# Performance work log

Measured on AMD Instinct MI355X. Metric: run time of the kernel, lower is better.

## Reference

```python
import jax, jax.numpy as jnp
import numpy as np

N, F_IN, C, H, L = 4096, 768, 256, 4, 2
DH = C // H  # 64 per-head dim for GATv2


def _ln(x, g, b, eps=1e-5):
    mu = x.mean(-1, keepdims=True)
    var = ((x - mu) ** 2).mean(-1, keepdims=True)
    return (x - mu) / jnp.sqrt(var + eps) * g + b


def _gat_layer(x, wl, wr, att, b, src, dst):
    # GATv2Conv: e_ij = att . leaky_relu(Wl x_j + Wr x_i); softmax over incoming j; concat heads.
    xs = (x @ wl).reshape(N, H, DH)  # source transform
    xd = (x @ wr).reshape(N, H, DH)  # target transform
    e = jnp.einsum('ehd,hd->eh', jax.nn.leaky_relu(xs[src] + xd[dst], 0.2), att)  # [E,H]
    m = jax.ops.segment_max(e, dst, num_segments=N)          # segment softmax (stable)
    p = jnp.exp(e - m[dst])
    s = jax.ops.segment_sum(p, dst, num_segments=N)
    alpha = p / (s[dst] + 1e-16)                             # [E,H]
    out = jax.ops.segment_sum(alpha[:, :, None] * xs[src], dst, num_segments=N)
    return out.reshape(N, C) + b


def _mha(x, wq, wk, wv, bq, bk, bv, wo, bo):
    # nn.MultiheadAttention, batch=1 sequence of all news nodes, eval mode.
    q = (x @ wq + bq).reshape(N, H, DH)
    k = (x @ wk + bk).reshape(N, H, DH)
    v = (x @ wv + bv).reshape(N, H, DH)
    scale = np.float32(1.0 / np.sqrt(DH))
    a = jax.nn.softmax(jnp.einsum('nhd,mhd->hnm', q, k) * scale, axis=-1)  # [H,N,N]
    o = jnp.einsum('hnm,mhd->nhd', a, v).reshape(N, C)
    return o @ wo + bo


def setup_inputs() -> dict:
    key = jax.random.key(0)
    ks = jax.random.split(key, 32)
    rn = lambda k, shp: (jax.random.normal(k, shp, dtype=jnp.float32) * 0.02)
    inp = {
        'x': jax.random.normal(ks[0], (N, F_IN), dtype=jnp.float32),
        'edge_index': jax.random.randint(ks[1], (2, N * 64), 0, N, dtype=jnp.int64),
        'emb_w': rn(ks[2], (F_IN, C)), 'emb_b': jnp.zeros((C,), jnp.float32),
        'g1_wl': rn(ks[3], (C, C)), 'g1_wr': rn(ks[4], (C, C)),
        'g1_att': rn(ks[5], (H, DH)), 'g1_b': jnp.zeros((C,), jnp.float32),
        'g2_wl': rn(ks[6], (C, C)), 'g2_wr': rn(ks[7], (C, C)),
        'g2_att': rn(ks[8], (H, DH)), 'g2_b': jnp.zeros((C,), jnp.float32),
        'mha_wq': rn(ks[9], (C, C)), 'mha_wk': rn(ks[10], (C, C)), 'mha_wv': rn(ks[11], (C, C)),
        'mha_bq': jnp.zeros((C,), jnp.float32), 'mha_bk': jnp.zeros((C,), jnp.float32),
        'mha_bv': jnp.zeros((C,), jnp.float32),
        'mha_wo': rn(ks[12], (C, C)), 'mha_bo': jnp.zeros((C,), jnp.float32),
        'ln_g': jnp.ones((C,), jnp.float32), 'ln_b': jnp.zeros((C,), jnp.float32),
        'cls_w1': rn(ks[13], (C, C // 2)), 'cls_b1': jnp.zeros((C // 2,), jnp.float32),
        'cls_w2': rn(ks[14], (C // 2, 2)), 'cls_b2': jnp.zeros((2,), jnp.float32),
    }
    return inp


def reference(x, edge_index, emb_w, emb_b, g1_wl, g1_wr, g1_att, g1_b,
              g2_wl, g2_wr, g2_att, g2_b, mha_wq, mha_wk, mha_wv, mha_bq,
              mha_bk, mha_bv, mha_wo, mha_bo, ln_g, ln_b,
              cls_w1, cls_b1, cls_w2, cls_b2):
    # add self loops (GATv2Conv default add_self_loops=True)
    loops = jnp.arange(N, dtype=edge_index.dtype)
    src = jnp.concatenate([edge_index[0], loops])
    dst = jnp.concatenate([edge_index[1], loops])

    h = x @ emb_w + emb_b                              # node embedding Linear(-1, C)
    h = jax.nn.relu(_gat_layer(h, g1_wl, g1_wr, g1_att, g1_b, src, dst))
    h = jax.nn.relu(_gat_layer(h, g2_wl, g2_wr, g2_att, g2_b, src, dst))

    # entity-aware self-attention + residual LayerNorm
    enh = _mha(h, mha_wq, mha_wk, mha_wv, mha_bq, mha_bk, mha_bv, mha_wo, mha_bo)
    h = _ln(h + enh, ln_g, ln_b)

    # classifier MLP (dropout = identity in eval)
    h = jax.nn.relu(h @ cls_w1 + cls_b1)
    return h @ cls_w2 + cls_b2
```

## Files before the change

kernel.cpp:

```cpp
#include <hip/hip_runtime.h>

typedef __attribute__((ext_vector_type(8))) short short8_t;
typedef __attribute__((ext_vector_type(4))) float f32x4_t;

#define N_NODES  4096
#define E0_EDGES 262144
#define E_TOTAL  266240
#define SPLITS   8
#define KV_PER_SPLIT (N_NODES / SPLITS)

__device__ __forceinline__ float bf2f(unsigned short u){
  union { unsigned int i; float f; } v; v.i = ((unsigned int)u) << 16; return v.f;
}
__device__ __forceinline__ unsigned short f2bf(float f){
  union { float f; unsigned int i; } v; v.f = f;
  unsigned int r = (v.i + 0x7FFFu + ((v.i >> 16) & 1u)) >> 16;
  return (unsigned short)r;
}
__device__ __forceinline__ unsigned int cvtpk_bf16(float lo, float hi){
  unsigned int r;
  asm volatile("v_cvt_pk_bf16_f32 %0, %1, %2" : "=v"(r) : "v"(lo), "v"(hi));
  return r;
}
template<int CTRL>
__device__ __forceinline__ float dpp_add(float x){
  int v = __builtin_amdgcn_update_dpp(0, __float_as_int(x), CTRL, 0xF, 0xF, true);
  return x + __int_as_float(v);
}
__device__ __forceinline__ float rowsum16(float x){
  x = dpp_add<0xB1>(x); x = dpp_add<0x4E>(x); x = dpp_add<0x124>(x); x = dpp_add<0x128>(x);
  return x;
}
__device__ __forceinline__ void wg_barrier(){
  asm volatile("s_waitcnt lgkmcnt(0)" ::: "memory");
  __builtin_amdgcn_s_barrier();
  asm volatile("" ::: "memory");
}

struct TJob { const float* src; unsigned short* dst; int rows, cols, tile0; };
struct TJobs { TJob j[10]; };

__global__ __launch_bounds__(256) void prep_kernel(const float* __restrict__ x, unsigned short* __restrict__ xb,
                                                   TJobs jobs, int tb, int* __restrict__ zp){
  __shared__ unsigned short tile[64 * 64];
  int b = blockIdx.x, t = threadIdx.x;
  if (b < 3072){
    int i = (b * 256 + t) * 4;
    float4 v = *(const float4*)&x[i];
    union { unsigned short u[4]; uint2 q; } o;
    o.u[0] = f2bf(v.x); o.u[1] = f2bf(v.y); o.u[2] = f2bf(v.z); o.u[3] = f2bf(v.w);
    *(uint2*)&xb[i] = o.q;
    return;
  }
  if (b < 3072 + tb){
    int bb = b - 3072;
    int ji = 0;
    #pragma unroll
    for (int k = 1; k < 10; k++) if (bb >= jobs.j[k].tile0) ji = k;
    TJob J = jobs.j[ji];
    int lt = bb - J.tile0;
    int tpr = J.cols >> 6;
    int tr = lt / tpr, tc = lt - tr * tpr;
    #pragma unroll
    for (int i2 = 0; i2 < 2; i2++){
      int e = i2 * 2048 + t * 8;
      int nl = e >> 6, c8 = e & 63;
      const float* sp = &J.src[(size_t)(tr * 64 + nl) * J.cols + tc * 64 + c8];
      float4 v0 = *(const float4*)sp;
      float4 v1 = *(const float4*)(sp + 4);
      union { unsigned short u[8]; uint4 q; } o;
      o.u[0]=f2bf(v0.x); o.u[1]=f2bf(v0.y); o.u[2]=f2bf(v0.z); o.u[3]=f2bf(v0.w);
      o.u[4]=f2bf(v1.x); o.u[5]=f2bf(v1.y); o.u[6]=f2bf(v1.z); o.u[7]=f2bf(v1.w);
      *(uint4*)&tile[nl * 64 + (((c8 >> 3) ^ ((nl >> 3) & 7)) * 8)] = o.q;
    }
    __syncthreads();
    #pragma unroll
    for (int i2 = 0; i2 < 2; i2++){
      int e = i2 * 2048 + t * 8;
      int cl = e >> 6, n8 = e & 63;
      union { unsigned short u[8]; uint4 q; } o;
      #pragma unroll
      for (int j = 0; j < 8; j++){
        int row = n8 + j;
        o.u[j] = tile[row * 64 + (((cl >> 3) ^ ((row >> 3) & 7)) * 8) + (cl & 7)];
      }
      *(uint4*)&J.dst[(size_t)(tc * 64 + cl) * J.rows + tr * 64 + n8] = o.q;
    }
    return;
  }
  int i = (b - 3072 - tb) * 256 + t;
  if (i < 8192) zp[i] = 0;
}

__global__ __launch_bounds__(256) void scatter_kernel(const int* __restrict__ ei, const int* __restrict__ offs,
                                                      int* __restrict__ cur, int* __restrict__ csrc){
  int e = blockIdx.x * 256 + threadIdx.x;
  if (e >= E_TOTAL) return;
  int s, d;
  if (e < E0_EDGES){ s = ei[e]; d = ei[E0_EDGES + e]; }
  else { s = d = e - E0_EDGES; }
  int pos = offs[d] + atomicAdd(&cur[d], 1);
  csrc[pos] = s;
}

struct GJob { const unsigned short* Wt; const float* bias; float* outF; unsigned short* outB; unsigned short* outT; };
struct GJobs { GJob j[3]; };
struct AuxJob { int mode; const int* ei; int* a; int* b; };

__global__ __launch_bounds__(256) void gemm_kernel(const unsigned short* __restrict__ A, GJobs jobs,
                                                   int K, int Nc, int relu, AuxJob AX){
  __shared__ unsigned short lds[8192];
  const int t = threadIdx.x;

  if (AX.mode && blockIdx.z == gridDim.z - 1){
    int flat = blockIdx.x + (blockIdx.y << 6);
    if (AX.mode == 1){
      for (int e = flat * 256 + t; e < E_TOTAL; e += 65536){
        int d = (e < E0_EDGES) ? AX.ei[E0_EDGES + e] : (e - E0_EDGES);
        atomicAdd(&AX.a[d], 1);
      }
    } else if (flat == 0){
      int* wtot = (int*)lds;
      int lane = t & 63, w = t >> 6;
      int v[16];
      int base = t * 16;
      int s = 0;
      #pragma unroll
      for (int j = 0; j < 16; j++){ v[j] = AX.a[base + j]; s += v[j]; }
      int x = s;
      #pragma unroll
      for (int off = 1; off < 64; off <<= 1){
        int y = __shfl_up(x, off, 64);
        if (lane >= off) x += y;
      }
      if (lane == 63) wtot[w] = x;
      __syncthreads();
      int wbase = 0;
      #pragma unroll
      for (int k = 0; k < 4; k++) if (k < w) wbase += wtot[k];
      int run = wbase + x - s;
      #pragma unroll
      for (int j = 0; j < 16; j++){ AX.b[base + j] = run; run += v[j]; }
      if (t == 255) AX.b[N_NODES] = run;
    }
    return;
  }

  const GJob job = jobs.j[blockIdx.z];
  const int lane = t & 63, w = t >> 6;
  const int wm = w >> 1, wn = w & 1;
  const int c16 = lane & 15, g = lane >> 4;
  const int bm = blockIdx.x, bn = blockIdx.y;

  const int srow = t >> 2, schunk = t & 3;
  const unsigned short* Ag = A      + (size_t)(bm * 64 + srow) * K + schunk * 8;
  const unsigned short* Bg = job.Wt + (size_t)(bn * 64 + srow) * K + schunk * 8;
  const int swz = srow * 32 + ((schunk ^ ((srow >> 1) & 3)) * 8);

  const int arow0 = wm * 32 + c16, arow1 = arow0 + 16;
  const int aoff0 = arow0 * 32 + ((g ^ ((arow0 >> 1) & 3)) * 8);
  const int aoff1 = arow1 * 32 + ((g ^ ((arow1 >> 1) & 3)) * 8);
  const int bcol0 = wn * 32 + c16, bcol1 = bcol0 + 16;
  const int boff0 = 2048 + bcol0 * 32 + ((g ^ ((bcol0 >> 1) & 3)) * 8);
  const int boff1 = 2048 + bcol1 * 32 + ((g ^ ((bcol1 >> 1) & 3)) * 8);

  f32x4_t acc[2][2] = {};
  const int nk = K >> 5;

  {
    uint4 av = *(const uint4*)(Ag);
    uint4 bv = *(const uint4*)(Bg);
    *(uint4*)&lds[swz]        = av;
    *(uint4*)&lds[2048 + swz] = bv;
  }
  int cur = 0;
  for (int i = 0; i < nk; i++){
    const bool pf = (i + 1) < nk;
    uint4 av, bv;
    if (pf){
      av = *(const uint4*)(Ag + (i + 1) * 32);
      bv = *(const uint4*)(Bg + (i + 1) * 32);
    }
    wg_barrier();
    const int base = cur * 4096;
    union { uint4 u; short8_t s; } a0, a1, b0, b1;
    a0.u = *(const uint4*)&lds[base + aoff0];
    a1.u = *(const uint4*)&lds[base + aoff1];
    b0.u = *(const uint4*)&lds[base + boff0];
    b1.u = *(const uint4*)&lds[base + boff1];
    acc[0][0] = __builtin_amdgcn_mfma_f32_16x16x32_bf16(a0.s, b0.s, acc[0][0], 0, 0, 0);
    acc[0][1] = __builtin_amdgcn_mfma_f32_16x16x32_bf16(a0.s, b1.s, acc[0][1], 0, 0, 0);
    acc[1][0] = __builtin_amdgcn_mfma_f32_16x16x32_bf16(a1.s, b0.s, acc[1][0], 0, 0, 0);
    acc[1][1] = __builtin_amdgcn_mfma_f32_16x16x32_bf16(a1.s, b1.s, acc[1][1], 0, 0, 0);
    if (pf){
      const int nb = (cur ^ 1) * 4096;
      *(uint4*)&lds[nb + swz]        = av;
      *(uint4*)&lds[nb + 2048 + swz] = bv;
      cur ^= 1;
    }
  }

  #pragma unroll
  for (int fm = 0; fm < 2; fm++){
    #pragma unroll
    for (int fn = 0; fn < 2; fn++){
      int col = bn * 64 + wn * 32 + fn * 16 + c16;
      float bia = job.bias ? job.bias[col] : 0.f;
      float vv[4];
      #pragma unroll
      for (int r = 0; r < 4; r++){
        float v = acc[fm][fn][r] + bia;
        if (relu) v = fmaxf(v, 0.f);
        vv[r] = v;
      }
      int row0 = bm * 64 + wm * 32 + fm * 16 + g * 4;
      if (job.outF){
        #pragma unroll
        for (int r = 0; r < 4; r++) job.outF[(size_t)(row0 + r) * Nc + col] = vv[r];
      }
      if (job.outB){
        #pragma unroll
        for (int r = 0; r < 4; r++) job.outB[(size_t)(row0 + r) * Nc + col] = f2bf(vv[r]);
      }
      if (job.outT){
        union { unsigned short u[4]; uint2 q; } pk;
        #pragma unroll
        for (int r = 0; r < 4; r++) pk.u[r] = f2bf(vv[r]);
        *(uint2*)&job.outT[(size_t)col * 4096 + row0] = pk.q;
      }
    }
  }
}

__global__ __launch_bounds__(256) void gat_gather(const unsigned short* __restrict__ xs, const unsigned short* __restrict__ xd,
                                                  const float* __restrict__ att, const float* __restrict__ bias,
                                                  const int* __restrict__ offs, const int* __restrict__ csrc,
                                                  unsigned short* __restrict__ outB, float* __restrict__ outF){
  __shared__ float combL[4][256];
  __shared__ float combS[4][4];
  const int i = blockIdx.x, t = threadIdx.x;
  const int lane = t & 63, w = t >> 6;
  float xdc[4], attc[4];
  {
    uint2 xv = *(const uint2*)&xd[i * 256 + lane * 4];
    xdc[0] = bf2f((unsigned short)(xv.x & 0xffff)); xdc[1] = bf2f((unsigned short)(xv.x >> 16));
    xdc[2] = bf2f((unsigned short)(xv.y & 0xffff)); xdc[3] = bf2f((unsigned short)(xv.y >> 16));
    float4 av = *(const float4*)&att[lane * 4];
    attc[0] = av.x; attc[1] = av.y; attc[2] = av.z; attc[3] = av.w;
  }
  const int b0 = offs[i], b1 = offs[i + 1];
  float acc0 = 0.f, acc1 = 0.f, acc2 = 0.f, acc3 = 0.f, ssum = 0.f;
  int p = b0 + w;
  for (; p + 4 < b1; p += 8){
    int sA = csrc[p], sB = csrc[p + 4];
    uint2 xa = *(const uint2*)&xs[sA * 256 + lane * 4];
    uint2 xb = *(const uint2*)&xs[sB * 256 + lane * 4];
    float a0 = bf2f((unsigned short)(xa.x & 0xffff)), a1 = bf2f((unsigned short)(xa.x >> 16));
    float a2 = bf2f((unsigned short)(xa.y & 0xffff)), a3 = bf2f((unsigned short)(xa.y >> 16));
    float b0_ = bf2f((unsigned short)(xb.x & 0xffff)), b1_ = bf2f((unsigned short)(xb.x >> 16));
    float b2_ = bf2f((unsigned short)(xb.y & 0xffff)), b3_ = bf2f((unsigned short)(xb.y >> 16));
    float va0 = a0 + xdc[0]; va0 = (va0 > 0.f) ? va0 : 0.2f * va0;
    float va1 = a1 + xdc[1]; va1 = (va1 > 0.f) ? va1 : 0.2f * va1;
    float va2 = a2 + xdc[2]; va2 = (va2 > 0.f) ? va2 : 0.2f * va2;
    float va3 = a3 + xdc[3]; va3 = (va3 > 0.f) ? va3 : 0.2f * va3;
    float vb0 = b0_ + xdc[0]; vb0 = (vb0 > 0.f) ? vb0 : 0.2f * vb0;
    float vb1 = b1_ + xdc[1]; vb1 = (vb1 > 0.f) ? vb1 : 0.2f * vb1;
    float vb2 = b2_ + xdc[2]; vb2 = (vb2 > 0.f) ? vb2 : 0.2f * vb2;
    float vb3 = b3_ + xdc[3]; vb3 = (vb3 > 0.f) ? vb3 : 0.2f * vb3;
    float eA = rowsum16(va0 * attc[0] + va1 * attc[1] + va2 * attc[2] + va3 * attc[3]);
    float eB = rowsum16(vb0 * attc[0] + vb1 * attc[1] + vb2 * attc[2] + vb3 * attc[3]);
    float pA = __expf(eA), pB = __expf(eB);
    ssum += pA + pB;
    acc0 += pA * a0 + pB * b0_; acc1 += pA * a1 + pB * b1_;
    acc2 += pA * a2 + pB * b2_; acc3 += pA * a3 + pB * b3_;
  }
  if (p < b1){
    int s = csrc[p];
    uint2 xv = *(const uint2*)&xs[s * 256 + lane * 4];
    float x0 = bf2f((unsigned short)(xv.x & 0xffff)), x1 = bf2f((unsigned short)(xv.x >> 16));
    float x2 = bf2f((unsigned short)(xv.y & 0xffff)), x3 = bf2f((unsigned short)(xv.y >> 16));
    float v0 = x0 + xdc[0]; v0 = (v0 > 0.f) ? v0 : 0.2f * v0;
    float v1 = x1 + xdc[1]; v1 = (v1 > 0.f) ? v1 : 0.2f * v1;
    float v2 = x2 + xdc[2]; v2 = (v2 > 0.f) ? v2 : 0.2f * v2;
    float v3 = x3 + xdc[3]; v3 = (v3 > 0.f) ? v3 : 0.2f * v3;
    float e = rowsum16(v0 * attc[0] + v1 * attc[1] + v2 * attc[2] + v3 * attc[3]);
    float pe = __expf(e);
    ssum += pe;
    acc0 += pe * x0; acc1 += pe * x1; acc2 += pe * x2; acc3 += pe * x3;
  }
  combL[w][lane * 4 + 0] = acc0; combL[w][lane * 4 + 1] = acc1;
  combL[w][lane * 4 + 2] = acc2; combL[w][lane * 4 + 3] = acc3;
  if ((lane & 15) == 0) combS[w][lane >> 4] = ssum;
  __syncthreads();
  float atot = combL[0][t] + combL[1][t] + combL[2][t] + combL[3][t];
  int hh = t >> 6;
  float stot = combS[0][hh] + combS[1][hh] + combS[2][hh] + combS[3][hh];
  float o = atot / (stot + 1e-16f) + bias[t];
  o = fmaxf(o, 0.f);
  outB[i * 256 + t] = f2bf(o);
  if (outF) outF[i * 256 + t] = o;
}

__global__ __launch_bounds__(512, 2) void attn_kernel(const unsigned short* __restrict__ qb, const unsigned short* __restrict__ kb,
                                                      const unsigned short* __restrict__ vt,
                                                      float* __restrict__ Opart, float* __restrict__ Ol){
  __shared__ unsigned short K_lds[2][4096];
  __shared__ unsigned short V_lds[2][4096];
  __shared__ unsigned short P_lds[8][2048];
  const int t = threadIdx.x, lane = t & 63, w = t >> 6;
  const int c16 = lane & 15, g = lane >> 4;
  const int h = blockIdx.y, bq = blockIdx.x, sp = blockIdx.z;

  const int sr = t >> 3, sc = (t & 7) * 8;
  const int kw = sr * 64 + (((t & 7) ^ ((sr >> 1) & 7)) * 8);
  const int vw = sr * 64 + (((t & 7) ^ (sr & 7)) * 8);

  short8_t qa[2][2];
  #pragma unroll
  for (int qm = 0; qm < 2; qm++){
    int qrow = bq * 256 + w * 32 + qm * 16 + c16;
    union { uint4 u; short8_t s; } cv0, cv1;
    cv0.u = *(const uint4*)&qb[(size_t)qrow * 256 + h * 64 + g * 8];
    cv1.u = *(const uint4*)&qb[(size_t)qrow * 256 + h * 64 + 32 + g * 8];
    qa[qm][0] = cv0.s; qa[qm][1] = cv1.s;
  }

  f32x4_t oacc[2][4] = {};
  float lsum[2] = {0.f, 0.f};

  const int kv_lo = sp * KV_PER_SPLIT;
  {
    uint4 k0 = *(const uint4*)&kb[(size_t)(kv_lo + sr) * 256 + h * 64 + sc];
    uint4 v0 = *(const uint4*)&vt[(size_t)(h * 64 + sr) * 4096 + kv_lo + sc];
    *(uint4*)&K_lds[0][kw] = k0;
    *(uint4*)&V_lds[0][vw] = v0;
  }
  int cur = 0;

  for (int ti = 0; ti < KV_PER_SPLIT / 64; ti++){
    const bool pf = (ti + 1) < KV_PER_SPLIT / 64;
    uint4 nk, nv;
    if (pf){
      int kvn = kv_lo + (ti + 1) * 64;
      nk = *(const uint4*)&kb[(size_t)(kvn + sr) * 256 + h * 64 + sc];
      nv = *(const uint4*)&vt[(size_t)(h * 64 + sr) * 4096 + kvn + sc];
    }
    wg_barrier();
    const unsigned short* Kb = K_lds[cur];
    const unsigned short* Vb = V_lds[cur];
    unsigned short* Pw = P_lds[w];

    f32x4_t sacc[2][4] = {};
    #pragma unroll
    for (int kd = 0; kd < 2; kd++){
      #pragma unroll
      for (int fn = 0; fn < 4; fn++){
        union { uint4 u; short8_t s; } kf;
        kf.u = *(const uint4*)&Kb[(fn * 16 + c16) * 64 + (((kd * 4 + g) ^ ((c16 >> 1) & 7)) * 8)];
        sacc[0][fn] = __builtin_amdgcn_mfma_f32_16x16x32_bf16(kf.s, qa[0][kd], sacc[0][fn], 0, 0, 0);
        sacc[1][fn] = __builtin_amdgcn_mfma_f32_16x16x32_bf16(kf.s, qa[1][kd], sacc[1][fn], 0, 0, 0);
      }
    }

    #pragma unroll
    for (int qm = 0; qm < 2; qm++){
      float ps = 0.f;
      int row = qm * 16 + c16;
      #pragma unroll
      for (int fn = 0; fn < 4; fn++){
        float p0 = __expf(sacc[qm][fn][0] * 0.125f);
        float p1 = __expf(sacc[qm][fn][1] * 0.125f);
        float p2 = __expf(sacc[qm][fn][2] * 0.125f);
        float p3 = __expf(sacc[qm][fn][3] * 0.125f);
        ps += (p0 + p1) + (p2 + p3);
        uint2 pk;
        pk.x = cvtpk_bf16(p0, p1);
        pk.y = cvtpk_bf16(p2, p3);
        int chunk = (fn * 2 + (g >> 1)) ^ (c16 & 7);
        *(uint2*)&Pw[row * 64 + chunk * 8 + (g & 1) * 4] = pk;
      }
      ps += __shfl_xor(ps, 16, 64);
      ps += __shfl_xor(ps, 32, 64);
      lsum[qm] += ps;
    }

    #pragma unroll
    for (int kd2 = 0; kd2 < 2; kd2++){
      const int ch = (((kd2 * 4 + g) ^ (c16 & 7)) * 8);
      union { uint4 u; short8_t s; } pt0, pt1;
      pt0.u = *(const uint4*)&Pw[c16 * 64 + ch];
      pt1.u = *(const uint4*)&Pw[(16 + c16) * 64 + ch];
      #pragma unroll
      for (int fn = 0; fn < 4; fn++){
        union { uint4 u; short8_t s; } vf;
        vf.u = *(const uint4*)&Vb[(fn * 16 + c16) * 64 + ch];
        oacc[0][fn] = __builtin_amdgcn_mfma_f32_16x16x32_bf16(vf.s, pt0.s, oacc[0][fn], 0, 0, 0);
        oacc[1][fn] = __builtin_amdgcn_mfma_f32_16x16x32_bf16(vf.s, pt1.s, oacc[1][fn], 0, 0, 0);
      }
    }

    if (pf){
      *(uint4*)&K_lds[cur ^ 1][kw] = nk;
      *(uint4*)&V_lds[cur ^ 1][vw] = nv;
      cur ^= 1;
    }
  }

  const int sh = sp * 4 + h;
  #pragma unroll
  for (int qm = 0; qm < 2; qm++){
    int node = bq * 256 + w * 32 + qm * 16 + c16;
    #pragma unroll
    for (int fn = 0; fn < 4; fn++){
      *(float4*)&Opart[((size_t)sh * N_NODES + node) * 64 + fn * 16 + g * 4] =
        *(float4*)&oacc[qm][fn];
    }
    if (g == 0) Ol[(size_t)sh * N_NODES + node] = lsum[qm];
  }
}

__global__ __launch_bounds__(256) void wo_ln_kernel(const float* __restrict__ Opart, const float* __restrict__ Ol,
                                                    const unsigned short* __restrict__ Wt, const float* __restrict__ bo,
                                                    const float* __restrict__ h2f, const float* __restrict__ gg,
                                                    const float* __restrict__ bb, unsigned short* __restrict__ outB){
  __shared__ unsigned short Ab[2][512];
  __shared__ unsigned short Bb[2][8192];
  __shared__ float red1[4][16], red2[4][16];
  __shared__ float Ls[64];
  const int t = threadIdx.x, lane = t & 63, w = t >> 6;
  const int c16 = lane & 15, g = lane >> 4;
  const int bm = blockIdx.x;

  const int arow = t >> 2, achk = t & 3;
  const int aswz = arow * 32 + ((achk ^ ((arow >> 1) & 3)) * 8);
  const int bq_ = t >> 2, bchk = t & 3;

  if (t < 64){
    int node = bm * 16 + (t >> 2), h = t & 3;
    float L = 0.f;
    #pragma unroll
    for (int s = 0; s < SPLITS; s++) L += Ol[(size_t)(s * 4 + h) * N_NODES + node];
    Ls[t] = 1.f / L;
  }
  __syncthreads();

  const int afr = c16 * 32 + ((g ^ ((c16 >> 1) & 3)) * 8);
  int bfr[4];
  #pragma unroll
  for (int fn = 0; fn < 4; fn++){
    int col = w * 64 + fn * 16 + c16;
    bfr[fn] = col * 32 + ((g ^ ((col >> 1) & 3)) * 8);
  }

  const int anode = bm * 16 + arow;
  auto loadA = [&](int k0, float4* pa){
    int c0 = k0 + achk * 8;
    int hh = c0 >> 6, d0 = c0 & 63;
    #pragma unroll
    for (int s = 0; s < SPLITS; s++){
      const float* bp = &Opart[((size_t)(s * 4 + hh) * N_NODES + anode) * 64 + d0];
      pa[s * 2]     = *(const float4*)bp;
      pa[s * 2 + 1] = *(const float4*)(bp + 4);
    }
  };
  auto packA = [&](int k0, const float4* pa) -> uint4 {
    float a[8] = {0.f,0.f,0.f,0.f,0.f,0.f,0.f,0.f};
    #pragma unroll
    for (int s = 0; s < SPLITS; s++){
      a[0] += pa[s*2].x;   a[1] += pa[s*2].y;   a[2] += pa[s*2].z;   a[3] += pa[s*2].w;
      a[4] += pa[s*2+1].x; a[5] += pa[s*2+1].y; a[6] += pa[s*2+1].z; a[7] += pa[s*2+1].w;
    }
    int c0 = k0 + achk * 8;
    float Li = Ls[(arow << 2) | (c0 >> 6)];
    union { unsigned short u[8]; uint4 q; } o;
    #pragma unroll
    for (int j = 0; j < 8; j++) o.u[j] = f2bf(a[j] * Li);
    return o.q;
  };

  f32x4_t acc[4] = {};
  {
    if (t < 64){
      float4 pa0[SPLITS * 2];
      loadA(0, pa0);
      *(uint4*)&Ab[0][aswz] = packA(0, pa0);
    }
    #pragma unroll
    for (int j = 0; j < 4; j++){
      int col = j * 64 + bq_;
      *(uint4*)&Bb[0][col * 32 + ((bchk ^ ((col >> 1) & 3)) * 8)] = *(const uint4*)&Wt[(size_t)col * 256 + bchk * 8];
    }
  }
  int cur = 0;
  for (int i = 0; i < 8; i++){
    const bool pf = i < 7;
    float4 pa[SPLITS * 2]; uint4 pb[4];
    int k1 = (i + 1) * 32;
    if (pf){
      if (t < 64) loadA(k1, pa);
      #pragma unroll
      for (int j = 0; j < 4; j++){
        int col = j * 64 + bq_;
        pb[j] = *(const uint4*)&Wt[(size_t)col * 256 + k1 + bchk * 8];
      }
    }
    wg_barrier();
    union { uint4 u; short8_t s; } a, b;
    a.u = *(const uint4*)&Ab[cur][afr];
    #pragma unroll
    for (int fn = 0; fn < 4; fn++){
      b.u = *(const uint4*)&Bb[cur][bfr[fn]];
      acc[fn] = __builtin_amdgcn_mfma_f32_16x16x32_bf16(a.s, b.s, acc[fn], 0, 0, 0);
    }
    if (pf){
      if (t < 64) *(uint4*)&Ab[cur ^ 1][aswz] = packA(k1, pa);
      #pragma unroll
      for (int j = 0; j < 4; j++){
        int col = j * 64 + bq_;
        *(uint4*)&Bb[cur ^ 1][col * 32 + ((bchk ^ ((col >> 1) & 3)) * 8)] = pb[j];
      }
      cur ^= 1;
    }
  }

  float vv[4][4];
  #pragma unroll
  for (int fn = 0; fn < 4; fn++){
    int col = w * 64 + fn * 16 + c16;
    float bia = bo[col];
    #pragma unroll
    for (int r = 0; r < 4; r++)
      vv[fn][r] = acc[fn][r] + bia + h2f[(size_t)(bm * 16 + g * 4 + r) * 256 + col];
  }
  #pragma unroll
  for (int r = 0; r < 4; r++){
    float a = 0.f, b = 0.f;
    #pragma unroll
    for (int fn = 0; fn < 4; fn++){ a += vv[fn][r]; b += vv[fn][r] * vv[fn][r]; }
    a = rowsum16(a); b = rowsum16(b);
    if (c16 == 0){ red1[w][g * 4 + r] = a; red2[w][g * 4 + r] = b; }
  }
  __syncthreads();
  #pragma unroll
  for (int r = 0; r < 4; r++){
    int row = g * 4 + r;
    float S1 = red1[0][row] + red1[1][row] + red1[2][row] + red1[3][row];
    float S2 = red2[0][row] + red2[1][row] + red2[2][row] + red2[3][row];
    float mean = S1 * (1.f / 256.f);
    float var = S2 * (1.f / 256.f) - mean * mean;
    float rs = rsqrtf(var + 1e-5f);
    #pragma unroll
    for (int fn = 0; fn < 4; fn++){
      int col = w * 64 + fn * 16 + c16;
      outB[(size_t)(bm * 16 + row) * 256 + col] = f2bf((vv[fn][r] - mean) * rs * gg[col] + bb[col]);
    }
  }
}

__global__ __launch_bounds__(256) void cls_kernel(const unsigned short* __restrict__ hln,
                                                  const unsigned short* __restrict__ Wt1, const float* __restrict__ b1,
                                                  const float* __restrict__ w2, const float* __restrict__ b2,
                                                  float* __restrict__ out){
  __shared__ unsigned short Ab[2][512];
  __shared__ unsigned short Bb[2][4096];
  __shared__ float red0[4][16], red1[4][16];
  const int t = threadIdx.x, lane = t & 63, w = t >> 6;
  const int c16 = lane & 15, g = lane >> 4;
  const int bm = blockIdx.x;

  const int arow = t >> 2, achk = t & 3;
  const unsigned short* Agp = hln + (size_t)(bm * 16 + arow) * 256 + achk * 8;
  const int aswz = arow * 32 + ((achk ^ ((arow >> 1) & 3)) * 8);
  const int bq_ = t >> 2, bchk = t & 3;

  const int afr = c16 * 32 + ((g ^ ((c16 >> 1) & 3)) * 8);
  int bfr[2];
  #pragma unroll
  for (int fn = 0; fn < 2; fn++){
    int col = w * 32 + fn * 16 + c16;
    bfr[fn] = col * 32 + ((g ^ ((col >> 1) & 3)) * 8);
  }

  f32x4_t acc[2] = {};
  {
    if (t < 64) *(uint4*)&Ab[0][aswz] = *(const uint4*)Agp;
    #pragma unroll
    for (int j = 0; j < 2; j++){
      int col = j * 64 + bq_;
      *(uint4*)&Bb[0][col * 32 + ((bchk ^ ((col >> 1) & 3)) * 8)] = *(const uint4*)&Wt1[(size_t)col * 256 + bchk * 8];
    }
  }
  int cur = 0;
  for (int i = 0; i < 8; i++){
    const bool pf = i < 7;
    uint4 pa; uint4 pb[2];
    if (pf){
      int k1 = (i + 1) * 32;
      if (t < 64) pa = *(const uint4*)(Agp + k1);
      #pragma unroll
      for (int j = 0; j < 2; j++){
        int col = j * 64 + bq_;
        pb[j] = *(const uint4*)&Wt1[(size_t)col * 256 + k1 + bchk * 8];
      }
    }
    wg_barrier();
    union { uint4 u; short8_t s; } a, b;
    a.u = *(const uint4*)&Ab[cur][afr];
    #pragma unroll
    for (int fn = 0; fn < 2; fn++){
      b.u = *(const uint4*)&Bb[cur][bfr[fn]];
      acc[fn] = __builtin_amdgcn_mfma_f32_16x16x32_bf16(a.s, b.s, acc[fn], 0, 0, 0);
    }
    if (pf){
      if (t < 64) *(uint4*)&Ab[cur ^ 1][aswz] = pa;
      #pragma unroll
      for (int j = 0; j < 2; j++){
        int col = j * 64 + bq_;
        *(uint4*)&Bb[cur ^ 1][col * 32 + ((bchk ^ ((col >> 1) & 3)) * 8)] = pb[j];
      }
      cur ^= 1;
    }
  }

  float vv[2][4];
  #pragma unroll
  for (int fn = 0; fn < 2; fn++){
    int col = w * 32 + fn * 16 + c16;
    float bia = b1[col];
    #pragma unroll
    for (int r = 0; r < 4; r++) vv[fn][r] = fmaxf(acc[fn][r] + bia, 0.f);
  }
  float w20 = w2[(w * 32 + c16) * 2],      w21 = w2[(w * 32 + c16) * 2 + 1];
  float w30 = w2[(w * 32 + 16 + c16) * 2], w31 = w2[(w * 32 + 16 + c16) * 2 + 1];
  #pragma unroll
  for (int r = 0; r < 4; r++){
    float a0 = vv[0][r] * w20 + vv[1][r] * w30;
    float a1 = vv[0][r] * w21 + vv[1][r] * w31;
    a0 = rowsum16(a0); a1 = rowsum16(a1);
    if (c16 == 0){ red0[w][g * 4 + r] = a0; red1[w][g * 4 + r] = a1; }
  }
  __syncthreads();
  if (t < 16){
    float q0 = red0[0][t] + red0[1][t] + red0[2][t] + red0[3][t] + b2[0];
    float q1 = red1[0][t] + red1[1][t] + red1[2][t] + red1[3][t] + b2[1];
    out[(size_t)(bm * 16 + t) * 2]     = q0;
    out[(size_t)(bm * 16 + t) * 2 + 1] = q1;
  }
}

extern "C" void kernel_launch(void* const* d_in, const int* in_sizes, int n_in,
                              void* d_out, int out_size, void* d_ws, size_t ws_size,
                              hipStream_t stream){
  const float* x      = (const float*)d_in[0];
  const int*   ei     = (const int*)d_in[1];
  const float* emb_w  = (const float*)d_in[2];
  const float* emb_b  = (const float*)d_in[3];
  const float* g1_wl  = (const float*)d_in[4];
  const float* g1_wr  = (const float*)d_in[5];
  const float* g1_att = (const float*)d_in[6];
  const float* g1_b   = (const float*)d_in[7];
  const float* g2_wl  = (const float*)d_in[8];
  const float* g2_wr  = (const float*)d_in[9];
  const float* g2_att = (const float*)d_in[10];
  const float* g2_b   = (const float*)d_in[11];
  const float* wq     = (const float*)d_in[12];
  const float* wk     = (const float*)d_in[13];
  const float* wv     = (const float*)d_in[14];
  const float* bq     = (const float*)d_in[15];
  const float* bk     = (const float*)d_in[16];
  const float* bv     = (const float*)d_in[17];
  const float* wo     = (const float*)d_in[18];
  const float* bo     = (const float*)d_in[19];
  const float* ln_g   = (const float*)d_in[20];
  const float* ln_b   = (const float*)d_in[21];
  const float* cls_w1 = (const float*)d_in[22];
  const float* cls_b1 = (const float*)d_in[23];
  const float* cls_w2 = (const float*)d_in[24];
  const float* cls_b2 = (const float*)d_in[25];
  float* out = (float*)d_out;

  char* wsb = (char*)d_ws;
  size_t o = 0;
  auto take = [&](size_t bytes) -> char* {
    char* r = wsb + o; o += (bytes + 255) & ~(size_t)255; return r;
  };
  unsigned short* wt_emb  = (unsigned short*)take(768 * 256 * 2);
  unsigned short* wt_wl1  = (unsigned short*)take(256 * 256 * 2);
  unsigned short* wt_wr1  = (unsigned short*)take(256 * 256 * 2);
  unsigned short* wt_wl2  = (unsigned short*)take(256 * 256 * 2);
  unsigned short* wt_wr2  = (unsigned short*)take(256 * 256 * 2);
  unsigned short* wt_wq   = (unsigned short*)take(256 * 256 * 2);
  unsigned short* wt_wk   = (unsigned short*)take(256 * 256 * 2);
  unsigned short* wt_wv   = (unsigned short*)take(256 * 256 * 2);
  unsigned short* wt_wo   = (unsigned short*)take(256 * 256 * 2);
  unsigned short* wt_cls1 = (unsigned short*)take(256 * 128 * 2);
  unsigned short* x_bf    = (unsigned short*)take((size_t)4096 * 768 * 2);
  unsigned short* h0_bf   = (unsigned short*)take((size_t)4096 * 256 * 2);
  unsigned short* xs1_bf  = (unsigned short*)take((size_t)4096 * 256 * 2);
  unsigned short* xd1_bf  = (unsigned short*)take((size_t)4096 * 256 * 2);
  unsigned short* h1_bf   = (unsigned short*)take((size_t)4096 * 256 * 2);
  unsigned short* xs2_bf  = (unsigned short*)take((size_t)4096 * 256 * 2);
  unsigned short* xd2_bf  = (unsigned short*)take((size_t)4096 * 256 * 2);
  unsigned short* h2_bf   = (unsigned short*)take((size_t)4096 * 256 * 2);
  float*          h2_f    = (float*)take((size_t)4096 * 256 * 4);
  unsigned short* q_bf    = (unsigned short*)take((size_t)4096 * 256 * 2);
  unsigned short* k_bf    = (unsigned short*)take((size_t)4096 * 256 * 2);
  unsigned short* vt_bf   = (unsigned short*)take((size_t)4096 * 256 * 2);
  unsigned short* hln_bf  = (unsigned short*)take((size_t)4096 * 256 * 2);
  int* deg  = (int*)take(4096 * 4);
  int* cur  = (int*)take(4096 * 4);
  int* offs = (int*)take(4097 * 4);
  int* csrc = (int*)take((size_t)E_TOTAL * 4);
  float* Opart = (float*)take((size_t)SPLITS * 4 * N_NODES * 64 * 4);
  float* Ol    = (float*)take((size_t)SPLITS * 4 * N_NODES * 4);

  TJobs TJ;
  TJob tj[10] = {
    { emb_w,  wt_emb,  768, 256, 0 },
    { g1_wl,  wt_wl1,  256, 256, 0 },
    { g1_wr,  wt_wr1,  256, 256, 0 },
    { g2_wl,  wt_wl2,  256, 256, 0 },
    { g2_wr,  wt_wr2,  256, 256, 0 },
    { wq,     wt_wq,   256, 256, 0 },
    { wk,     wt_wk,   256, 256, 0 },
    { wv,     wt_wv,   256, 256, 0 },
    { wo,     wt_wo,   256, 256, 0 },
    { cls_w1, wt_cls1, 256, 128, 0 },
  };
  int tb = 0;
  for (int i = 0; i < 10; i++){
    tj[i].tile0 = tb;
    tb += (tj[i].rows >> 6) * (tj[i].cols >> 6);
    TJ.j[i] = tj[i];
  }
  prep_kernel<<<3072 + tb + 32, 256, 0, stream>>>(x, x_bf, TJ, tb, deg);

  GJobs J;
  AuxJob AX0 = { 0, nullptr, nullptr, nullptr };
  J = {}; J.j[0] = { wt_emb, emb_b, nullptr, h0_bf, nullptr };
  AuxJob AXh = { 1, ei, deg, nullptr };
  gemm_kernel<<<dim3(64, 4, 2), 256, 0, stream>>>(x_bf, J, 768, 256, 0, AXh);
  J = {}; J.j[0] = { wt_wl1, nullptr, nullptr, xs1_bf, nullptr }; J.j[1] = { wt_wr1, nullptr, nullptr, xd1_bf, nullptr };
  AuxJob AXs = { 2, nullptr, deg, offs };
  gemm_kernel<<<dim3(64, 4, 3), 256, 0, stream>>>(h0_bf, J, 256, 256, 0, AXs);
  scatter_kernel<<<(E_TOTAL + 255) / 256, 256, 0, stream>>>(ei, offs, cur, csrc);
  gat_gather<<<4096, 256, 0, stream>>>(xs1_bf, xd1_bf, g1_att, g1_b, offs, csrc, h1_bf, nullptr);
  J = {}; J.j[0] = { wt_wl2, nullptr, nullptr, xs2_bf, nullptr }; J.j[1] = { wt_wr2, nullptr, nullptr, xd2_bf, nullptr };
  gemm_kernel<<<dim3(64, 4, 2), 256, 0, stream>>>(h1_bf, J, 256, 256, 0, AX0);
  gat_gather<<<4096, 256, 0, stream>>>(xs2_bf, xd2_bf, g2_att, g2_b, offs, csrc, h2_bf, h2_f);
  J = {};
  J.j[0] = { wt_wq, bq, nullptr, q_bf, nullptr };
  J.j[1] = { wt_wk, bk, nullptr, k_bf, nullptr };
  J.j[2] = { wt_wv, bv, nullptr, nullptr, vt_bf };
  gemm_kernel<<<dim3(64, 4, 3), 256, 0, stream>>>(h2_bf, J, 256, 256, 0, AX0);
  attn_kernel<<<dim3(16, 4, SPLITS), 512, 0, stream>>>(q_bf, k_bf, vt_bf, Opart, Ol);
  wo_ln_kernel<<<256, 256, 0, stream>>>(Opart, Ol, wt_wo, bo, h2_f, ln_g, ln_b, hln_bf);
  cls_kernel<<<256, 256, 0, stream>>>(hln_bf, wt_cls1, cls_b1, cls_w2, cls_b2, out);

  (void)in_sizes; (void)n_in; (void)out_size; (void)ws_size;
}
```

Measured before the change: 164.1 us.

## Keep attention probabilities in registers, fold Q scale, fuse LN with classifier

The attention kernel now feeds the bf16 probabilities straight from registers into 16x16x16 MFMAs instead of staging them through LDS. The block shrinks to 256 threads with 128 query rows each, and the 1/sqrt(d) scale is moved into the Q projection epilogue. The Wo+LayerNorm kernel is fused with the classifier MLP, keeping the normalized rows in LDS instead of a global round trip and dropping one launch. The narrower K=16 MFMA issues more instructions, and halving the query tile means each K/V tile is reused across fewer queries.

```diff
diff --git a/kernel.cpp b/kernel.cpp
--- a/kernel.cpp
+++ b/kernel.cpp
@@ -1,6 +1,7 @@
 #include <hip/hip_runtime.h>
 
 typedef __attribute__((ext_vector_type(8))) short short8_t;
+typedef __attribute__((ext_vector_type(4))) short short4_t;
 typedef __attribute__((ext_vector_type(4))) float f32x4_t;
 
 #define N_NODES  4096
@@ -35,6 +36,10 @@
   asm volatile("s_waitcnt lgkmcnt(0)" ::: "memory");
   __builtin_amdgcn_s_barrier();
   asm volatile("" ::: "memory");
+}
+__device__ __forceinline__ f32x4_t mfma16(short4_t a, short4_t b, f32x4_t c){
+  asm("v_mfma_f32_16x16x16_bf16 %0, %1, %2, %0" : "+v"(c) : "v"(a), "v"(b));
+  return c;
 }
 
 struct TJob { const float* src; unsigned short* dst; int rows, cols, tile0; };
@@ -103,7 +108,7 @@
   csrc[pos] = s;
 }
 
-struct GJob { const unsigned short* Wt; const float* bias; float* outF; unsigned short* outB; unsigned short* outT; };
+struct GJob { const unsigned short* Wt; const float* bias; float* outF; unsigned short* outB; unsigned short* outT; float scale; };
 struct GJobs { GJob j[3]; };
 struct AuxJob { int mode; const int* ei; int* a; int* b; };
 
@@ -209,7 +214,7 @@
       float vv[4];
       #pragma unroll
       for (int r = 0; r < 4; r++){
-        float v = acc[fm][fn][r] + bia;
+        float v = (acc[fm][fn][r] + bia) * job.scale;
         if (relu) v = fmaxf(v, 0.f);
         vv[r] = v;
       }
@@ -301,24 +306,27 @@
   if (outF) outF[i * 256 + t] = o;
 }
 
-__global__ __launch_bounds__(512, 2) void attn_kernel(const unsigned short* __restrict__ qb, const unsigned short* __restrict__ kb,
+__global__ __launch_bounds__(256, 4) void attn_kernel(const unsigned short* __restrict__ qb, const unsigned short* __restrict__ kb,
                                                       const unsigned short* __restrict__ vt,
                                                       float* __restrict__ Opart, float* __restrict__ Ol){
   __shared__ unsigned short K_lds[2][4096];
   __shared__ unsigned short V_lds[2][4096];
-  __shared__ unsigned short P_lds[8][2048];
   const int t = threadIdx.x, lane = t & 63, w = t >> 6;
   const int c16 = lane & 15, g = lane >> 4;
   const int h = blockIdx.y, bq = blockIdx.x, sp = blockIdx.z;
 
-  const int sr = t >> 3, sc = (t & 7) * 8;
-  const int kw = sr * 64 + (((t & 7) ^ ((sr >> 1) & 7)) * 8);
-  const int vw = sr * 64 + (((t & 7) ^ (sr & 7)) * 8);
+  const int e0 = t * 8, e1 = 2048 + t * 8;
+  const int sr0 = e0 >> 6, sc0 = e0 & 63;
+  const int sr1 = e1 >> 6, sc1 = e1 & 63;
+  const int kw0 = sr0 * 64 + (((sc0 >> 3) ^ ((sr0 >> 1) & 7)) * 8);
+  const int kw1 = sr1 * 64 + (((sc1 >> 3) ^ ((sr1 >> 1) & 7)) * 8);
+  const int vw0 = sr0 * 64 + (((sc0 >> 3) ^ (sr0 & 7)) * 8);
+  const int vw1 = sr1 * 64 + (((sc1 >> 3) ^ (sr1 & 7)) * 8);
 
   short8_t qa[2][2];
   #pragma unroll
   for (int qm = 0; qm < 2; qm++){
-    int qrow = bq * 256 + w * 32 + qm * 16 + c16;
+    int qrow = bq * 128 + w * 32 + qm * 16 + c16;
     union { uint4 u; short8_t s; } cv0, cv1;
     cv0.u = *(const uint4*)&qb[(size_t)qrow * 256 + h * 64 + g * 8];
     cv1.u = *(const uint4*)&qb[(size_t)qrow * 256 + h * 64 + 32 + g * 8];
@@ -330,25 +338,28 @@
 
   const int kv_lo = sp * KV_PER_SPLIT;
   {
-    uint4 k0 = *(const uint4*)&kb[(size_t)(kv_lo + sr) * 256 + h * 64 + sc];
-    uint4 v0 = *(const uint4*)&vt[(size_t)(h * 64 + sr) * 4096 + kv_lo + sc];
-    *(uint4*)&K_lds[0][kw] = k0;
-    *(uint4*)&V_lds[0][vw] = v0;
+    uint4 k0 = *(const uint4*)&kb[(size_t)(kv_lo + sr0) * 256 + h * 64 + sc0];
+    uint4 k1 = *(const uint4*)&kb[(size_t)(kv_lo + sr1) * 256 + h * 64 + sc1];
+    uint4 v0 = *(const uint4*)&vt[(size_t)(h * 64 + sr0) * 4096 + kv_lo + sc0];
+    uint4 v1 = *(const uint4*)&vt[(size_t)(h * 64 + sr1) * 4096 + kv_lo + sc1];
+    *(uint4*)&K_lds[0][kw0] = k0; *(uint4*)&K_lds[0][kw1] = k1;
+    *(uint4*)&V_lds[0][vw0] = v0; *(uint4*)&V_lds[0][vw1] = v1;
   }
   int cur = 0;
 
   for (int ti = 0; ti < KV_PER_SPLIT / 64; ti++){
     const bool pf = (ti + 1) < KV_PER_SPLIT / 64;
-    uint4 nk, nv;
+    uint4 nk0, nk1, nv0, nv1;
     if (pf){
       int kvn = kv_lo + (ti + 1) * 64;
-      nk = *(const uint4*)&kb[(size_t)(kvn + sr) * 256 + h * 64 + sc];
-      nv = *(const uint4*)&vt[(size_t)(h * 64 + sr) * 4096 + kvn + sc];
+      nk0 = *(const uint4*)&kb[(size_t)(kvn + sr0) * 256 + h * 64 + sc0];
+      nk1 = *(const uint4*)&kb[(size_t)(kvn + sr1) * 256 + h * 64 + sc1];
+      nv0 = *(const uint4*)&vt[(size_t)(h * 64 + sr0) * 4096 + kvn + sc0];
+      nv1 = *(const uint4*)&vt[(size_t)(h * 64 + sr1) * 4096 + kvn + sc1];
     }
     wg_barrier();
     const unsigned short* Kb = K_lds[cur];
     const unsigned short* Vb = V_lds[cur];
-    unsigned short* Pw = P_lds[w];
 
     f32x4_t sacc[2][4] = {};
     #pragma unroll
@@ -362,22 +373,21 @@
       }
     }
 
+    short4_t pfr[2][4];
     #pragma unroll
     for (int qm = 0; qm < 2; qm++){
       float ps = 0.f;
-      int row = qm * 16 + c16;
       #pragma unroll
       for (int fn = 0; fn < 4; fn++){
-        float p0 = __expf(sacc[qm][fn][0] * 0.125f);
-        float p1 = __expf(sacc[qm][fn][1] * 0.125f);
-        float p2 = __expf(sacc[qm][fn][2] * 0.125f);
-        float p3 = __expf(sacc[qm][fn][3] * 0.125f);
+        float p0 = __expf(sacc[qm][fn][0]);
+        float p1 = __expf(sacc[qm][fn][1]);
+        float p2 = __expf(sacc[qm][fn][2]);
+        float p3 = __expf(sacc[qm][fn][3]);
         ps += (p0 + p1) + (p2 + p3);
-        uint2 pk;
-        pk.x = cvtpk_bf16(p0, p1);
-        pk.y = cvtpk_bf16(p2, p3);
-        int chunk = (fn * 2 + (g >> 1)) ^ (c16 & 7);
-        *(uint2*)&Pw[row * 64 + chunk * 8 + (g & 1) * 4] = pk;
+        union { uint2 u; short4_t s; } pk;
+        pk.u.x = cvtpk_bf16(p0, p1);
+        pk.u.y = cvtpk_bf16(p2, p3);
+        pfr[qm][fn] = pk.s;
       }
       ps += __shfl_xor(ps, 16, 64);
       ps += __shfl_xor(ps, 32, 64);
@@ -385,23 +395,21 @@
     }
 
     #pragma unroll
-    for (int kd2 = 0; kd2 < 2; kd2++){
-      const int ch = (((kd2 * 4 + g) ^ (c16 & 7)) * 8);
-      union { uint4 u; short8_t s; } pt0, pt1;
-      pt0.u = *(const uint4*)&Pw[c16 * 64 + ch];
-      pt1.u = *(const uint4*)&Pw[(16 + c16) * 64 + ch];
-      #pragma unroll
-      for (int fn = 0; fn < 4; fn++){
-        union { uint4 u; short8_t s; } vf;
-        vf.u = *(const uint4*)&Vb[(fn * 16 + c16) * 64 + ch];
-        oacc[0][fn] = __builtin_amdgcn_mfma_f32_16x16x32_bf16(vf.s, pt0.s, oacc[0][fn], 0, 0, 0);
-        oacc[1][fn] = __builtin_amdgcn_mfma_f32_16x16x32_bf16(vf.s, pt1.s, oacc[1][fn], 0, 0, 0);
+    for (int fnkv = 0; fnkv < 4; fnkv++){
+      const int chb = fnkv * 2 + (g >> 1);
+      #pragma unroll
+      for (int fd = 0; fd < 4; fd++){
+        int row = fd * 16 + c16;
+        union { uint2 u; short4_t s; } vf;
+        vf.u = *(const uint2*)&Vb[row * 64 + ((chb ^ (row & 7)) * 8) + (g & 1) * 4];
+        oacc[0][fd] = mfma16(vf.s, pfr[0][fnkv], oacc[0][fd]);
+        oacc[1][fd] = mfma16(vf.s, pfr[1][fnkv], oacc[1][fd]);
       }
     }
 
     if (pf){
-      *(uint4*)&K_lds[cur ^ 1][kw] = nk;
-      *(uint4*)&V_lds[cur ^ 1][vw] = nv;
+      *(uint4*)&K_lds[cur ^ 1][kw0] = nk0; *(uint4*)&K_lds[cur ^ 1][kw1] = nk1;
+      *(uint4*)&V_lds[cur ^ 1][vw0] = nv0; *(uint4*)&V_lds[cur ^ 1][vw1] = nv1;
       cur ^= 1;
     }
   }
@@ -409,23 +417,29 @@
   const int sh = sp * 4 + h;
   #pragma unroll
   for (int qm = 0; qm < 2; qm++){
-    int node = bq * 256 + w * 32 + qm * 16 + c16;
-    #pragma unroll
-    for (int fn = 0; fn < 4; fn++){
-      *(float4*)&Opart[((size_t)sh * N_NODES + node) * 64 + fn * 16 + g * 4] =
-        *(float4*)&oacc[qm][fn];
+    int node = bq * 128 + w * 32 + qm * 16 + c16;
+    #pragma unroll
+    for (int fd = 0; fd < 4; fd++){
+      *(float4*)&Opart[((size_t)sh * N_NODES + node) * 64 + fd * 16 + g * 4] =
+        *(float4*)&oacc[qm][fd];
     }
     if (g == 0) Ol[(size_t)sh * N_NODES + node] = lsum[qm];
   }
 }
 
-__global__ __launch_bounds__(256) void wo_ln_kernel(const float* __restrict__ Opart, const float* __restrict__ Ol,
-                                                    const unsigned short* __restrict__ Wt, const float* __restrict__ bo,
-                                                    const float* __restrict__ h2f, const float* __restrict__ gg,
-                                                    const float* __restrict__ bb, unsigned short* __restrict__ outB){
+__global__ __launch_bounds__(256) void wo_ln_cls_kernel(const float* __restrict__ Opart, const float* __restrict__ Ol,
+                                                        const unsigned short* __restrict__ Wt, const float* __restrict__ bo,
+                                                        const float* __restrict__ h2f, const float* __restrict__ gg,
+                                                        const float* __restrict__ bb,
+                                                        const unsigned short* __restrict__ Wt1, const float* __restrict__ b1,
+                                                        const float* __restrict__ w2, const float* __restrict__ b2,
+                                                        float* __restrict__ out){
   __shared__ unsigned short Ab[2][512];
   __shared__ unsigned short Bb[2][8192];
+  __shared__ unsigned short Cb[2][4096];
+  __shared__ unsigned short hl[16 * 264];
   __shared__ float red1[4][16], red2[4][16];
+  __shared__ float cred0[4][16], cred1[4][16];
   __shared__ float Ls[64];
   const int t = threadIdx.x, lane = t & 63, w = t >> 6;
   const int c16 = lane & 15, g = lane >> 4;
@@ -552,51 +566,31 @@
     #pragma unroll
     for (int fn = 0; fn < 4; fn++){
       int col = w * 64 + fn * 16 + c16;
-      outB[(size_t)(bm * 16 + row) * 256 + col] = f2bf((vv[fn][r] - mean) * rs * gg[col] + bb[col]);
-    }
-  }
-}
-
-__global__ __launch_bounds__(256) void cls_kernel(const unsigned short* __restrict__ hln,
-                                                  const unsigned short* __restrict__ Wt1, const float* __restrict__ b1,
-                                                  const float* __restrict__ w2, const float* __restrict__ b2,
-                                                  float* __restrict__ out){
-  __shared__ unsigned short Ab[2][512];
-  __shared__ unsigned short Bb[2][4096];
-  __shared__ float red0[4][16], red1[4][16];
-  const int t = threadIdx.x, lane = t & 63, w = t >> 6;
-  const int c16 = lane & 15, g = lane >> 4;
-  const int bm = blockIdx.x;
-
-  const int arow = t >> 2, achk = t & 3;
-  const unsigned short* Agp = hln + (size_t)(bm * 16 + arow) * 256 + achk * 8;
-  const int aswz = arow * 32 + ((achk ^ ((arow >> 1) & 3)) * 8);
-  const int bq_ = t >> 2, bchk = t & 3;
-
-  const int afr = c16 * 32 + ((g ^ ((c16 >> 1) & 3)) * 8);
-  int bfr[2];
+      hl[row * 264 + col] = f2bf((vv[fn][r] - mean) * rs * gg[col] + bb[col]);
+    }
+  }
+
+  wg_barrier();
+  int cfr[2];
   #pragma unroll
   for (int fn = 0; fn < 2; fn++){
     int col = w * 32 + fn * 16 + c16;
-    bfr[fn] = col * 32 + ((g ^ ((col >> 1) & 3)) * 8);
-  }
-
-  f32x4_t acc[2] = {};
+    cfr[fn] = col * 32 + ((g ^ ((col >> 1) & 3)) * 8);
+  }
+  f32x4_t cacc[2] = {};
   {
-    if (t < 64) *(uint4*)&Ab[0][aswz] = *(const uint4*)Agp;
     #pragma unroll
     for (int j = 0; j < 2; j++){
       int col = j * 64 + bq_;
-      *(uint4*)&Bb[0][col * 32 + ((bchk ^ ((col >> 1) & 3)) * 8)] = *(const uint4*)&Wt1[(size_t)col * 256 + bchk * 8];
-    }
-  }
-  int cur = 0;
+      *(uint4*)&Cb[0][col * 32 + ((bchk ^ ((col >> 1) & 3)) * 8)] = *(const uint4*)&Wt1[(size_t)col * 256 + bchk * 8];
+    }
+  }
+  cur = 0;
   for (int i = 0; i < 8; i++){
     const bool pf = i < 7;
-    uint4 pa; uint4 pb[2];
+    uint4 pb[2];
     if (pf){
       int k1 = (i + 1) * 32;
-      if (t < 64) pa = *(const uint4*)(Agp + k1);
       #pragma unroll
       for (int j = 0; j < 2; j++){
         int col = j * 64 + bq_;
@@ -605,44 +599,42 @@
     }
     wg_barrier();
     union { uint4 u; short8_t s; } a, b;
-    a.u = *(const uint4*)&Ab[cur][afr];
+    a.u = *(const uint4*)&hl[c16 * 264 + i * 32 + g * 8];
     #pragma unroll
     for (int fn = 0; fn < 2; fn++){
-      b.u = *(const uint4*)&Bb[cur][bfr[fn]];
-      acc[fn] = __builtin_amdgcn_mfma_f32_16x16x32_bf16(a.s, b.s, acc[fn], 0, 0, 0);
+      b.u = *(const uint4*)&Cb[cur][cfr[fn]];
+      cacc[fn] = __builtin_amdgcn_mfma_f32_16x16x32_bf16(a.s, b.s, cacc[fn], 0, 0, 0);
     }
     if (pf){
-      if (t < 64) *(uint4*)&Ab[cur ^ 1][aswz] = pa;
       #pragma unroll
       for (int j = 0; j < 2; j++){
         int col = j * 64 + bq_;
-        *(uint4*)&Bb[cur ^ 1][col * 32 + ((bchk ^ ((col >> 1) & 3)) * 8)] = pb[j];
+        *(uint4*)&Cb[cur ^ 1][col * 32 + ((bchk ^ ((col >> 1) & 3)) * 8)] = pb[j];
       }
       cur ^= 1;
     }
   }
-
-  float vv[2][4];
+  float cv[2][4];
   #pragma unroll
   for (int fn = 0; fn < 2; fn++){
     int col = w * 32 + fn * 16 + c16;
     float bia = b1[col];
     #pragma unroll
-    for (int r = 0; r < 4; r++) vv[fn][r] = fmaxf(acc[fn][r] + bia, 0.f);
+    for (int r = 0; r < 4; r++) cv[fn][r] = fmaxf(cacc[fn][r] + bia, 0.f);
   }
   float w20 = w2[(w * 32 + c16) * 2],      w21 = w2[(w * 32 + c16) * 2 + 1];
   float w30 = w2[(w * 32 + 16 + c16) * 2], w31 = w2[(w * 32 + 16 + c16) * 2 + 1];
   #pragma unroll
   for (int r = 0; r < 4; r++){
-    float a0 = vv[0][r] * w20 + vv[1][r] * w30;
-    float a1 = vv[0][r] * w21 + vv[1][r] * w31;
+    float a0 = cv[0][r] * w20 + cv[1][r] * w30;
+    float a1 = cv[0][r] * w21 + cv[1][r] * w31;
     a0 = rowsum16(a0); a1 = rowsum16(a1);
-    if (c16 == 0){ red0[w][g * 4 + r] = a0; red1[w][g * 4 + r] = a1; }
+    if (c16 == 0){ cred0[w][g * 4 + r] = a0; cred1[w][g * 4 + r] = a1; }
   }
   __syncthreads();
   if (t < 16){
-    float q0 = red0[0][t] + red0[1][t] + red0[2][t] + red0[3][t] + b2[0];
-    float q1 = red1[0][t] + red1[1][t] + red1[2][t] + red1[3][t] + b2[1];
+    float q0 = cred0[0][t] + cred0[1][t] + cred0[2][t] + cred0[3][t] + b2[0];
+    float q1 = cred1[0][t] + cred1[1][t] + cred1[2][t] + cred1[3][t] + b2[1];
     out[(size_t)(bm * 16 + t) * 2]     = q0;
     out[(size_t)(bm * 16 + t) * 2 + 1] = q1;
   }
@@ -706,7 +698,6 @@
   unsigned short* q_bf    = (unsigned short*)take((size_t)4096 * 256 * 2);
   unsigned short* k_bf    = (unsigned short*)take((size_t)4096 * 256 * 2);
   unsigned short* vt_bf   = (unsigned short*)take((size_t)4096 * 256 * 2);
-  unsigned short* hln_bf  = (unsigned short*)take((size_t)4096 * 256 * 2);
   int* deg  = (int*)take(4096 * 4);
   int* cur  = (int*)take(4096 * 4);
   int* offs = (int*)take(4097 * 4);
@@ -737,25 +728,25 @@
 
   GJobs J;
   AuxJob AX0 = { 0, nullptr, nullptr, nullptr };
-  J = {}; J.j[0] = { wt_emb, emb_b, nullptr, h0_bf, nullptr };
+  J = {}; J.j[0] = { wt_emb, emb_b, nullptr, h0_bf, nullptr, 1.f };
   AuxJob AXh = { 1, ei, deg, nullptr };
   gemm_kernel<<<dim3(64, 4, 2), 256, 0, stream>>>(x_bf, J, 768, 256, 0, AXh);
-  J = {}; J.j[0] = { wt_wl1, nullptr, nullptr, xs1_bf, nullptr }; J.j[1] = { wt_wr1, nullptr, nullptr, xd1_bf, nullptr };
+  J = {}; J.j[0] = { wt_wl1, nullptr, nullptr, xs1_bf, nullptr, 1.f }; J.j[1] = { wt_wr1, nullptr, nullptr, xd1_bf, nullptr, 1.f };
   AuxJob AXs = { 2, nullptr, deg, offs };
   gemm_kernel<<<dim3(64, 4, 3), 256, 0, stream>>>(h0_bf, J, 256, 256, 0, AXs);
   scatter_kernel<<<(E_TOTAL + 255) / 256, 256, 0, stream>>>(ei, offs, cur, csrc);
   gat_gather<<<4096, 256, 0, stream>>>(xs1_bf, xd1_bf, g1_att, g1_b, offs, csrc, h1_bf, nullptr);
-  J = {}; J.j[0] = { wt_wl2, nullptr, nullptr, xs2_bf, nullptr }; J.j[1] = { wt_wr2, nullptr, nullptr, xd2_bf, nullptr };
+  J = {}; J.j[0] = { wt_wl2, nullptr, nullptr, xs2_bf, nullptr, 1.f }; J.j[1] = { wt_wr2, nullptr, nullptr, xd2_bf, nullptr, 1.f };
   gemm_kernel<<<dim3(64, 4, 2), 256, 0, stream>>>(h1_bf, J, 256, 256, 0, AX0);
   gat_gather<<<4096, 256, 0, stream>>>(xs2_bf, xd2_bf, g2_att, g2_b, offs, csrc, h2_bf, h2_f);
   J = {};
-  J.j[0] = { wt_wq, bq, nullptr, q_bf, nullptr };
-  J.j[1] = { wt_wk, bk, nullptr, k_bf, nullptr };
-  J.j[2] = { wt_wv, bv, nullptr, nullptr, vt_bf };
+  J.j[0] = { wt_wq, bq, nullptr, q_bf, nullptr, 0.125f };
+  J.j[1] = { wt_wk, bk, nullptr, k_bf, nullptr, 1.f };
+  J.j[2] = { wt_wv, bv, nullptr, nullptr, vt_bf, 1.f };
   gemm_kernel<<<dim3(64, 4, 3), 256, 0, stream>>>(h2_bf, J, 256, 256, 0, AX0);
-  attn_kernel<<<dim3(16, 4, SPLITS), 512, 0, stream>>>(q_bf, k_bf, vt_bf, Opart, Ol);
-  wo_ln_kernel<<<256, 256, 0, stream>>>(Opart, Ol, wt_wo, bo, h2_f, ln_g, ln_b, hln_bf);
-  cls_kernel<<<256, 256, 0, stream>>>(hln_bf, wt_cls1, cls_b1, cls_w2, cls_b2, out);
+  attn_kernel<<<dim3(32, 4, SPLITS), 256, 0, stream>>>(q_bf, k_bf, vt_bf, Opart, Ol);
+  wo_ln_cls_kernel<<<256, 256, 0, stream>>>(Opart, Ol, wt_wo, bo, h2_f, ln_g, ln_b,
+                                            wt_cls1, cls_b1, cls_w2, cls_b2, out);
 
   (void)in_sizes; (void)n_in; (void)out_size; (void)ws_size;
 }
```

Result: slower. 173.3 us (+5.6%).
